# Kernel optimization log

Measured on AMD Instinct MI355X. Metric: run time of the kernel, lower is better.

## Reference

```python
import jax, jax.numpy as jnp
import numpy as np

# Standard asymmetric NF4 value table (bitsandbytes / flute nf_utils, bits=4, symmetric=False)
NF4_VALUES = np.array([
    -1.0, -0.6961928009986877, -0.5250730514526367, -0.39491748809814453,
    -0.28444138169288635, -0.18477343022823334, -0.09105003625154495, 0.0,
    0.07958029955625534, 0.16093020141124725, 0.2461123913526535,
    0.33791524171829224, 0.44070982933044434, 0.5626170039176941,
    0.7229568362236023, 1.0], dtype=np.float32)
# Pivots are midpoints between consecutive values -> nearest-value bucketing via searchsorted
NF4_PIVOTS = (NF4_VALUES[:-1] + NF4_VALUES[1:]) / 2.0

GROUP_SIZE = 64
IN_FEATURES = 4096
OUT_FEATURES = 4096
BATCH, SEQ = 4, 2048


def setup_inputs() -> dict:
    key = jax.random.key(0)
    k1, k2 = jax.random.split(key)
    inp = jax.random.normal(k1, (BATCH, SEQ, IN_FEATURES), dtype=jnp.float32)
    weight = jax.random.normal(k2, (OUT_FEATURES, IN_FEATURES), dtype=jnp.float32) * 0.02
    # scales initialized exactly as in __init__: per-group absmax of the weight
    scales = jnp.max(jnp.abs(weight.reshape(-1, GROUP_SIZE)), axis=1, keepdims=True)  # [out*in/64, 1]
    return {
        "inp": inp,
        "weight": weight,
        "scales": scales,
        "values": jnp.asarray(NF4_VALUES),
        "pivots": jnp.asarray(NF4_PIVOTS),
    }


def _manual_nf4(weight, scales, values, pivots, group_size):
    # groupwise absmax-normalize, nearest-value lookup via pivot search, dequantize
    w = weight.reshape(-1, group_size)                 # [n_groups, group_size]
    scaled = jnp.clip(w / scales, -1.0, 1.0)
    idx = jnp.searchsorted(pivots, scaled)             # nearest NF4 code
    qweight = values[idx] * scales                     # dequantized bf16-style weight
    return qweight.reshape(weight.shape)


def reference(inp, weight, scales, values, pivots):
    qweight = _manual_nf4(weight, scales, values, pivots, GROUP_SIZE)  # [out, in]
    # F.linear(inp, qweight), bias=None
    return jnp.einsum('bsi,oi->bso', inp, qweight)
```

## Files before the change

### kernel.cpp

```cpp
#include <hip/hip_runtime.h>
#include <hip/hip_bf16.h>
#include <stdint.h>

#define M_DIM 8192
#define N_DIM 4096
#define K_DIM 4096
#define BM 256
#define BN 256
#define BK 64
#define NT (K_DIM / BK)

#define CVT_BLOCKS 8192
#define DQ_BLOCKS  8192

typedef float f32x16 __attribute__((ext_vector_type(16)));
typedef __bf16 bf16x8 __attribute__((ext_vector_type(8)));
typedef short s16x8 __attribute__((ext_vector_type(8)));

template <typename AB>
__device__ __forceinline__ auto mfma_32x32x16(AB a, AB b, f32x16 c, int)
    -> decltype(__builtin_amdgcn_mfma_f32_32x32x16_bf16(a, b, c, 0, 0, 0)) {
  return __builtin_amdgcn_mfma_f32_32x32x16_bf16(a, b, c, 0, 0, 0);
}
template <typename AB>
__device__ __forceinline__ f32x16 mfma_32x32x16(AB a, AB b, f32x16 c, long) {
  return __builtin_amdgcn_mfma_f32_32x32x16_bf16(
      __builtin_bit_cast(s16x8, a), __builtin_bit_cast(s16x8, b), c, 0, 0, 0);
}

__device__ __forceinline__ uint16_t f2b(float f) {
  union { float f; uint32_t u; } v; v.f = f;
  uint32_t u = v.u;
  u += 0x7FFFu + ((u >> 16) & 1u);
  return (uint16_t)(u >> 16);
}

__global__ __launch_bounds__(256) void prep(const float* __restrict__ inp,
                                            uint16_t* __restrict__ A_bf16,
                                            const float* __restrict__ w,
                                            const float* __restrict__ scales,
                                            const float* __restrict__ values,
                                            const float* __restrict__ pivots,
                                            uint16_t* __restrict__ B_bf16) {
  if (blockIdx.x < CVT_BLOCKS) {
    size_t t = (size_t)blockIdx.x * blockDim.x + threadIdx.x;
    const float4* p = (const float4*)inp + t * 4;
    uint4* q = (uint4*)A_bf16 + t * 2;
#pragma unroll
    for (int h = 0; h < 2; ++h) {
      float4 a = p[2 * h], b = p[2 * h + 1];
      uint4 o;
      o.x = (uint32_t)f2b(a.x) | ((uint32_t)f2b(a.y) << 16);
      o.y = (uint32_t)f2b(a.z) | ((uint32_t)f2b(a.w) << 16);
      o.z = (uint32_t)f2b(b.x) | ((uint32_t)f2b(b.y) << 16);
      o.w = (uint32_t)f2b(b.z) | ((uint32_t)f2b(b.w) << 16);
      q[h] = o;
    }
  } else {
    __shared__ float sv[16];
    if (threadIdx.x < 16) sv[threadIdx.x] = values[threadIdx.x];
    float pv[15];
#pragma unroll
    for (int j = 0; j < 15; ++j) pv[j] = pivots[j];
    __syncthreads();
    size_t t = (size_t)(blockIdx.x - CVT_BLOCKS) * blockDim.x + threadIdx.x;
    size_t base = t * 8;
    float scale = scales[base >> 6];
    float psc[15];
#pragma unroll
    for (int j = 0; j < 15; ++j) psc[j] = pv[j] * scale;
    const float4* p = (const float4*)(w + base);
    float4 a = p[0], b = p[1];
    float e[8] = {a.x, a.y, a.z, a.w, b.x, b.y, b.z, b.w};
    uint32_t words[4];
#pragma unroll
    for (int i = 0; i < 4; ++i) {
      uint32_t hw[2];
#pragma unroll
      for (int h = 0; h < 2; ++h) {
        float x = e[2 * i + h];
        int idx = 0;
#pragma unroll
        for (int j = 0; j < 15; ++j) idx += (psc[j] < x) ? 1 : 0;
        hw[h] = f2b(sv[idx] * scale);
      }
      words[i] = hw[0] | (hw[1] << 16);
    }
    uint4 o = {words[0], words[1], words[2], words[3]};
    ((uint4*)B_bf16)[t] = o;
  }
}


#define GLL(SRC, LOFF)                                                        \
  __builtin_amdgcn_global_load_lds(                                           \
      (__attribute__((address_space(1))) void*)(void*)(SRC),                  \
      (__attribute__((address_space(3))) void*)(smem + (LOFF)), 16, 0, 0)

#define STAGE_A(NB, KH, KEL)                                                  \
  do {                                                                        \
    GLL(Ab + gs0 + (KEL) + (KH) * 32, (NB) * 32768u + (KH) * 16384u + l0);    \
    GLL(Ab + gs1 + (KEL) + (KH) * 32, (NB) * 32768u + (KH) * 16384u + l1);    \
  } while (0)
#define STAGE_B(NB, KH, KEL)                                                  \
  do {                                                                        \
    GLL(Bb + gs0 + (KEL) + (KH) * 32,                                         \
        65536u + (NB) * 32768u + (KH) * 16384u + l0);                         \
    GLL(Bb + gs1 + (KEL) + (KH) * 32,                                         \
        65536u + (NB) * 32768u + (KH) * 16384u + l1);                         \
  } while (0)

#define MIDBAR()                                                              \
  do {                                                                        \
    asm volatile("" ::: "memory");                                            \
    __builtin_amdgcn_s_barrier();                                             \
    __builtin_amdgcn_sched_barrier(0);                                        \
  } while (0)
#define VM4BAR()                                                              \
  do {                                                                        \
    asm volatile("s_waitcnt vmcnt(4)" ::: "memory");                          \
    __builtin_amdgcn_s_barrier();                                             \
    __builtin_amdgcn_sched_barrier(0);                                        \
  } while (0)

#define PHASE0(CUR, NB, KH, KEL)                                              \
  do {                                                                        \
    const uint32_t _ab = (CUR) * 32768u + (KH) * 16384u + aoff;               \
    const uint32_t _bb = 65536u + (CUR) * 32768u + (KH) * 16384u + boff;      \
    bf16x8 a00 = *(const bf16x8*)(smem + _ab + cb0);                          \
    bf16x8 a10 = *(const bf16x8*)(smem + _ab + 2048u + cb0);                  \
    bf16x8 a01 = *(const bf16x8*)(smem + _ab + cb1);                          \
    bf16x8 a11 = *(const bf16x8*)(smem + _ab + 2048u + cb1);                  \
    b00 = *(const bf16x8*)(smem + _bb + cb0);                                 \
    b10 = *(const bf16x8*)(smem + _bb + 2048u + cb0);                         \
    b01 = *(const bf16x8*)(smem + _bb + cb1);                                 \
    b11 = *(const bf16x8*)(smem + _bb + 2048u + cb1);                         \
    STAGE_A(NB, KH, KEL);                                                     \
    MIDBAR();                                                                 \
    __builtin_amdgcn_s_setprio(1);                                            \
    acc[0][0] = mfma_32x32x16(a00, b00, acc[0][0], 0);                        \
    acc[0][1] = mfma_32x32x16(a00, b10, acc[0][1], 0);                        \
    acc[1][0] = mfma_32x32x16(a10, b00, acc[1][0], 0);                        \
    acc[1][1] = mfma_32x32x16(a10, b10, acc[1][1], 0);                        \
    acc[0][0] = mfma_32x32x16(a01, b01, acc[0][0], 0);                        \
    acc[0][1] = mfma_32x32x16(a01, b11, acc[0][1], 0);                        \
    acc[1][0] = mfma_32x32x16(a11, b01, acc[1][0], 0);                        \
    acc[1][1] = mfma_32x32x16(a11, b11, acc[1][1], 0);                        \
    __builtin_amdgcn_sched_barrier(0);                                        \
    __builtin_amdgcn_s_setprio(0);                                            \
    MIDBAR();                                                                 \
  } while (0)

#define PHASE1(CUR, NB, KH, KEL)                                              \
  do {                                                                        \
    const uint32_t _ab = (CUR) * 32768u + (KH) * 16384u + aoff + 4096u;       \
    bf16x8 a00 = *(const bf16x8*)(smem + _ab + cb0);                          \
    bf16x8 a10 = *(const bf16x8*)(smem + _ab + 2048u + cb0);                  \
    bf16x8 a01 = *(const bf16x8*)(smem + _ab + cb1);                          \
    bf16x8 a11 = *(const bf16x8*)(smem + _ab + 2048u + cb1);                  \
    STAGE_B(NB, KH, KEL);                                                     \
    MIDBAR();                                                                 \
    __builtin_amdgcn_s_setprio(1);                                            \
    acc[2][0] = mfma_32x32x16(a00, b00, acc[2][0], 0);                        \
    acc[2][1] = mfma_32x32x16(a00, b10, acc[2][1], 0);                        \
    acc[3][0] = mfma_32x32x16(a10, b00, acc[3][0], 0);                        \
    acc[3][1] = mfma_32x32x16(a10, b10, acc[3][1], 0);                        \
    acc[2][0] = mfma_32x32x16(a01, b01, acc[2][0], 0);                        \
    acc[2][1] = mfma_32x32x16(a01, b11, acc[2][1], 0);                        \
    acc[3][0] = mfma_32x32x16(a11, b01, acc[3][0], 0);                        \
    acc[3][1] = mfma_32x32x16(a11, b11, acc[3][1], 0);                        \
    __builtin_amdgcn_sched_barrier(0);                                        \
    __builtin_amdgcn_s_setprio(0);                                            \
    VM4BAR();                                                                 \
  } while (0)

__global__ __launch_bounds__(512, 2) void gemm_bt(const uint16_t* __restrict__ A,
                                                  const uint16_t* __restrict__ B,
                                                  float* __restrict__ C) {
  __shared__ char smem[131072];
  const int tid = threadIdx.x;
  const int wave = tid >> 6;
  const int lane = tid & 63;

  const int bid = blockIdx.x;
  const int wg = (bid & 7) * 64 + (bid >> 3);
  const int bm = wg >> 4;
  const int bn = wg & 15;

  const int wm = wave >> 2;
  const int wn = wave & 3;
  const int r31 = lane & 31;
  const int hi = lane >> 5;

  const int swz = (r31 >> 1) & 3;
  const uint32_t cb0 = (uint32_t)(((hi ^ swz) * 16));
  const uint32_t cb1 = (uint32_t)((((2 + hi) ^ swz) * 16));
  const uint32_t aoff = (uint32_t)(wm * 8192 + r31 * 64);
  const uint32_t boff = (uint32_t)(wn * 4096 + r31 * 64);

  const int s0 = wave * 128 + lane;
  const int r0 = s0 >> 2;
  const uint32_t gs0 =
      (uint32_t)r0 * K_DIM + (uint32_t)((((s0 & 3) ^ ((r0 >> 1) & 3)) * 8));
  const int s1 = s0 + 64;
  const int r1 = s1 >> 2;
  const uint32_t gs1 =
      (uint32_t)r1 * K_DIM + (uint32_t)((((s1 & 3) ^ ((r1 >> 1) & 3)) * 8));
  const uint32_t l0 = (uint32_t)(wave * 2048);
  const uint32_t l1 = l0 + 1024u;

  const uint16_t* Ab = A + (size_t)bm * BM * K_DIM;
  const uint16_t* Bb = B + (size_t)bn * BN * K_DIM;

  f32x16 acc[4][2] = {};

  STAGE_A(0u, 0u, 0u);
  STAGE_B(0u, 0u, 0u);
  STAGE_A(0u, 1u, 0u);
  STAGE_B(0u, 1u, 0u);
  asm volatile("s_waitcnt vmcnt(4)" ::: "memory");
  __builtin_amdgcn_s_barrier();
  __builtin_amdgcn_sched_barrier(0);

  for (int kt2 = 0; kt2 < NT; kt2 += 2) {
    const uint32_t kel0 = (uint32_t)(kt2 + 1) * BK;
    const uint32_t kel1 =
        (uint32_t)((kt2 + 2 < NT) ? (kt2 + 2) : (NT - 1)) * BK;
    {
      bf16x8 b00, b10, b01, b11;
      PHASE0(0u, 1u, 0u, kel0);
      PHASE1(0u, 1u, 0u, kel0);
      PHASE0(0u, 1u, 1u, kel0);
      PHASE1(0u, 1u, 1u, kel0);
    }
    {
      bf16x8 b00, b10, b01, b11;
      PHASE0(1u, 0u, 0u, kel1);
      PHASE1(1u, 0u, 0u, kel1);
      PHASE0(1u, 0u, 1u, kel1);
      PHASE1(1u, 0u, 1u, kel1);
    }
  }

  asm volatile("s_waitcnt vmcnt(0)" ::: "memory");

  const int crow0 = bm * BM + wm * 128;
  const int ccol0 = bn * BN + wn * 64 + r31;
#pragma unroll
  for (int i = 0; i < 4; ++i)
#pragma unroll
    for (int j = 0; j < 2; ++j)
#pragma unroll
      for (int reg = 0; reg < 16; ++reg) {
        int row = i * 32 + (reg & 3) + 8 * (reg >> 2) + 4 * hi;
        C[(size_t)(crow0 + row) * N_DIM + ccol0 + j * 32] = acc[i][j][reg];
      }
}

extern "C" void kernel_launch(void* const* d_in, const int* in_sizes, int n_in,
                              void* d_out, int out_size, void* d_ws, size_t ws_size,
                              hipStream_t stream) {
  const float* inp    = (const float*)d_in[0];
  const float* weight = (const float*)d_in[1];
  const float* scales = (const float*)d_in[2];
  const float* values = (const float*)d_in[3];
  const float* pivots = (const float*)d_in[4];
  float* out = (float*)d_out;

  uint16_t* A_bf16 = (uint16_t*)d_ws;
  uint16_t* B_bf16 = A_bf16 + (size_t)M_DIM * K_DIM;

  prep<<<CVT_BLOCKS + DQ_BLOCKS, 256, 0, stream>>>(inp, A_bf16, weight, scales, values,
                                                   pivots, B_bf16);
  gemm_bt<<<dim3(512), 512, 0, stream>>>(A_bf16, B_bf16, out);
}
```

Measured before the change: 546.3 us.

## Restructure GEMM main loop to cut barriers and split LDS reads by k-chunk

Measured after the change: 520.5 us. 1.05x faster.

```diff
diff --git a/kernel.cpp b/kernel.cpp
--- a/kernel.cpp
+++ b/kernel.cpp
@@ -43,18 +43,17 @@
                                             const float* __restrict__ pivots,
                                             uint16_t* __restrict__ B_bf16) {
   if (blockIdx.x < CVT_BLOCKS) {
-    size_t t = (size_t)blockIdx.x * blockDim.x + threadIdx.x;
-    const float4* p = (const float4*)inp + t * 4;
-    uint4* q = (uint4*)A_bf16 + t * 2;
-#pragma unroll
-    for (int h = 0; h < 2; ++h) {
-      float4 a = p[2 * h], b = p[2 * h + 1];
-      uint4 o;
+    size_t t0 = (size_t)blockIdx.x * 256 + threadIdx.x;
+    const float4* pin = (const float4*)inp;
+    uint2* pout = (uint2*)A_bf16;
+#pragma unroll
+    for (int it = 0; it < 4; ++it) {
+      size_t i = t0 + (size_t)it * ((size_t)CVT_BLOCKS * 256);
+      float4 a = pin[i];
+      uint2 o;
       o.x = (uint32_t)f2b(a.x) | ((uint32_t)f2b(a.y) << 16);
       o.y = (uint32_t)f2b(a.z) | ((uint32_t)f2b(a.w) << 16);
-      o.z = (uint32_t)f2b(b.x) | ((uint32_t)f2b(b.y) << 16);
-      o.w = (uint32_t)f2b(b.z) | ((uint32_t)f2b(b.w) << 16);
-      q[h] = o;
+      pout[i] = o;
     }
   } else {
     __shared__ float sv[16];
@@ -63,31 +62,29 @@
 #pragma unroll
     for (int j = 0; j < 15; ++j) pv[j] = pivots[j];
     __syncthreads();
-    size_t t = (size_t)(blockIdx.x - CVT_BLOCKS) * blockDim.x + threadIdx.x;
-    size_t base = t * 8;
-    float scale = scales[base >> 6];
-    float psc[15];
-#pragma unroll
-    for (int j = 0; j < 15; ++j) psc[j] = pv[j] * scale;
-    const float4* p = (const float4*)(w + base);
-    float4 a = p[0], b = p[1];
-    float e[8] = {a.x, a.y, a.z, a.w, b.x, b.y, b.z, b.w};
-    uint32_t words[4];
-#pragma unroll
-    for (int i = 0; i < 4; ++i) {
-      uint32_t hw[2];
-#pragma unroll
-      for (int h = 0; h < 2; ++h) {
-        float x = e[2 * i + h];
+    size_t t0 = (size_t)(blockIdx.x - CVT_BLOCKS) * 256 + threadIdx.x;
+    const float4* pw = (const float4*)w;
+    uint2* pout = (uint2*)B_bf16;
+#pragma unroll
+    for (int it = 0; it < 2; ++it) {
+      size_t i = t0 + (size_t)it * ((size_t)DQ_BLOCKS * 256);
+      float scale = scales[i >> 4];
+      float psc[15];
+#pragma unroll
+      for (int j = 0; j < 15; ++j) psc[j] = pv[j] * scale;
+      float4 a = pw[i];
+      float e[4] = {a.x, a.y, a.z, a.w};
+      uint32_t hw[4];
+#pragma unroll
+      for (int k = 0; k < 4; ++k) {
         int idx = 0;
 #pragma unroll
-        for (int j = 0; j < 15; ++j) idx += (psc[j] < x) ? 1 : 0;
-        hw[h] = f2b(sv[idx] * scale);
+        for (int j = 0; j < 15; ++j) idx += (psc[j] < e[k]) ? 1 : 0;
+        hw[k] = f2b(sv[idx] * scale);
       }
-      words[i] = hw[0] | (hw[1] << 16);
+      uint2 o = {hw[0] | (hw[1] << 16), hw[2] | (hw[3] << 16)};
+      pout[i] = o;
     }
-    uint4 o = {words[0], words[1], words[2], words[3]};
-    ((uint4*)B_bf16)[t] = o;
   }
 }
 
@@ -110,68 +107,63 @@
         65536u + (NB) * 32768u + (KH) * 16384u + l1);                         \
   } while (0)
 
-#define MIDBAR()                                                              \
-  do {                                                                        \
-    asm volatile("" ::: "memory");                                            \
-    __builtin_amdgcn_s_barrier();                                             \
-    __builtin_amdgcn_sched_barrier(0);                                        \
-  } while (0)
-#define VM4BAR()                                                              \
+#define SYNC4()                                                               \
   do {                                                                        \
     asm volatile("s_waitcnt vmcnt(4)" ::: "memory");                          \
     __builtin_amdgcn_s_barrier();                                             \
     __builtin_amdgcn_sched_barrier(0);                                        \
   } while (0)
 
-#define PHASE0(CUR, NB, KH, KEL)                                              \
+#define READ6(A0, A1, A2, A3, B0, B1, CUR, KH, CB)                            \
   do {                                                                        \
     const uint32_t _ab = (CUR) * 32768u + (KH) * 16384u + aoff;               \
     const uint32_t _bb = 65536u + (CUR) * 32768u + (KH) * 16384u + boff;      \
-    bf16x8 a00 = *(const bf16x8*)(smem + _ab + cb0);                          \
-    bf16x8 a10 = *(const bf16x8*)(smem + _ab + 2048u + cb0);                  \
-    bf16x8 a01 = *(const bf16x8*)(smem + _ab + cb1);                          \
-    bf16x8 a11 = *(const bf16x8*)(smem + _ab + 2048u + cb1);                  \
-    b00 = *(const bf16x8*)(smem + _bb + cb0);                                 \
-    b10 = *(const bf16x8*)(smem + _bb + 2048u + cb0);                         \
-    b01 = *(const bf16x8*)(smem + _bb + cb1);                                 \
-    b11 = *(const bf16x8*)(smem + _bb + 2048u + cb1);                         \
+    A0 = *(const bf16x8*)(smem + _ab + (CB));                                 \
+    A1 = *(const bf16x8*)(smem + _ab + 2048u + (CB));                         \
+    A2 = *(const bf16x8*)(smem + _ab + 4096u + (CB));                         \
+    A3 = *(const bf16x8*)(smem + _ab + 6144u + (CB));                         \
+    B0 = *(const bf16x8*)(smem + _bb + (CB));                                 \
+    B1 = *(const bf16x8*)(smem + _bb + 2048u + (CB));                         \
+  } while (0)
+
+#define MFMA8(A0, A1, A2, A3, B0, B1)                                         \
+  do {                                                                        \
+    acc[0][0] = mfma_32x32x16(A0, B0, acc[0][0], 0);                          \
+    acc[0][1] = mfma_32x32x16(A0, B1, acc[0][1], 0);                          \
+    acc[1][0] = mfma_32x32x16(A1, B0, acc[1][0], 0);                          \
+    acc[1][1] = mfma_32x32x16(A1, B1, acc[1][1], 0);                          \
+    acc[2][0] = mfma_32x32x16(A2, B0, acc[2][0], 0);                          \
+    acc[2][1] = mfma_32x32x16(A2, B1, acc[2][1], 0);                          \
+    acc[3][0] = mfma_32x32x16(A3, B0, acc[3][0], 0);                          \
+    acc[3][1] = mfma_32x32x16(A3, B1, acc[3][1], 0);                          \
+  } while (0)
+
+#define HALF(CUR, NB, KH, KEL)                                                \
+  do {                                                                        \
+    bf16x8 xa0, xa1, xa2, xa3, xb0, xb1;                                      \
+    bf16x8 ya0, ya1, ya2, ya3, yb0, yb1;                                      \
+    READ6(xa0, xa1, xa2, xa3, xb0, xb1, CUR, KH, cb0);                        \
+    READ6(ya0, ya1, ya2, ya3, yb0, yb1, CUR, KH, cb1);                        \
     STAGE_A(NB, KH, KEL);                                                     \
-    MIDBAR();                                                                 \
+    asm volatile("s_waitcnt lgkmcnt(6)" ::: "memory");                        \
+    __builtin_amdgcn_sched_barrier(0);                                        \
     __builtin_amdgcn_s_setprio(1);                                            \
-    acc[0][0] = mfma_32x32x16(a00, b00, acc[0][0], 0);                        \
-    acc[0][1] = mfma_32x32x16(a00, b10, acc[0][1], 0);                        \
-    acc[1][0] = mfma_32x32x16(a10, b00, acc[1][0], 0);                        \
-    acc[1][1] = mfma_32x32x16(a10, b10, acc[1][1], 0);                        \
-    acc[0][0] = mfma_32x32x16(a01, b01, acc[0][0], 0);                        \
-    acc[0][1] = mfma_32x32x16(a01, b11, acc[0][1], 0);                        \
-    acc[1][0] = mfma_32x32x16(a11, b01, acc[1][0], 0);                        \
-    acc[1][1] = mfma_32x32x16(a11, b11, acc[1][1], 0);                        \
+    MFMA8(xa0, xa1, xa2, xa3, xb0, xb1);                                      \
+    __builtin_amdgcn_s_setprio(0);                                            \
+    STAGE_B(NB, KH, KEL);                                                     \
+    asm volatile("s_waitcnt lgkmcnt(0)" ::: "memory");                        \
     __builtin_amdgcn_sched_barrier(0);                                        \
+    __builtin_amdgcn_s_setprio(1);                                            \
+    MFMA8(ya0, ya1, ya2, ya3, yb0, yb1);                                      \
     __builtin_amdgcn_s_setprio(0);                                            \
-    MIDBAR();                                                                 \
-  } while (0)
-
-#define PHASE1(CUR, NB, KH, KEL)                                              \
-  do {                                                                        \
-    const uint32_t _ab = (CUR) * 32768u + (KH) * 16384u + aoff + 4096u;       \
-    bf16x8 a00 = *(const bf16x8*)(smem + _ab + cb0);                          \
-    bf16x8 a10 = *(const bf16x8*)(smem + _ab + 2048u + cb0);                  \
-    bf16x8 a01 = *(const bf16x8*)(smem + _ab + cb1);                          \
-    bf16x8 a11 = *(const bf16x8*)(smem + _ab + 2048u + cb1);                  \
-    STAGE_B(NB, KH, KEL);                                                     \
-    MIDBAR();                                                                 \
-    __builtin_amdgcn_s_setprio(1);                                            \
-    acc[2][0] = mfma_32x32x16(a00, b00, acc[2][0], 0);                        \
-    acc[2][1] = mfma_32x32x16(a00, b10, acc[2][1], 0);                        \
-    acc[3][0] = mfma_32x32x16(a10, b00, acc[3][0], 0);                        \
-    acc[3][1] = mfma_32x32x16(a10, b10, acc[3][1], 0);                        \
-    acc[2][0] = mfma_32x32x16(a01, b01, acc[2][0], 0);                        \
-    acc[2][1] = mfma_32x32x16(a01, b11, acc[2][1], 0);                        \
-    acc[3][0] = mfma_32x32x16(a11, b01, acc[3][0], 0);                        \
-    acc[3][1] = mfma_32x32x16(a11, b11, acc[3][1], 0);                        \
-    __builtin_amdgcn_sched_barrier(0);                                        \
-    __builtin_amdgcn_s_setprio(0);                                            \
-    VM4BAR();                                                                 \
+  } while (0)
+
+#define TILE(CUR, NB, KEL)                                                    \
+  do {                                                                        \
+    HALF(CUR, NB, 0u, KEL);                                                   \
+    SYNC4();                                                                  \
+    HALF(CUR, NB, 1u, KEL);                                                   \
+    SYNC4();                                                                  \
   } while (0)
 
 __global__ __launch_bounds__(512, 2) void gemm_bt(const uint16_t* __restrict__ A,
@@ -226,20 +218,8 @@
     const uint32_t kel0 = (uint32_t)(kt2 + 1) * BK;
     const uint32_t kel1 =
         (uint32_t)((kt2 + 2 < NT) ? (kt2 + 2) : (NT - 1)) * BK;
-    {
-      bf16x8 b00, b10, b01, b11;
-      PHASE0(0u, 1u, 0u, kel0);
-      PHASE1(0u, 1u, 0u, kel0);
-      PHASE0(0u, 1u, 1u, kel0);
-      PHASE1(0u, 1u, 1u, kel0);
-    }
-    {
-      bf16x8 b00, b10, b01, b11;
-      PHASE0(1u, 0u, 0u, kel1);
-      PHASE1(1u, 0u, 0u, kel1);
-      PHASE0(1u, 0u, 1u, kel1);
-      PHASE1(1u, 0u, 1u, kel1);
-    }
+    TILE(0u, 1u, kel0);
+    TILE(1u, 0u, kel1);
   }
 
   asm volatile("s_waitcnt vmcnt(0)" ::: "memory");
```
